# Performance work log

Measured on AMD Instinct MI355X. Metric: run time of the kernel, lower is better.

The kernel has to match this reference:

```python
import jax, jax.numpy as jnp
import numpy as np

N = 100000   # nodes
E = 1600000  # edges
C = 128      # channels
EPS = 1e-5   # BatchNorm eps (PyG gnn.BatchNorm default)


def gcn_conv(x, W, b, src, dst, n):
    """PyG GCNConv: linear -> sym-normalized aggregation with self-loops -> bias."""
    h = x @ W                                      # [N, C]
    # degree with self-loops: in-degree at dst + 1
    deg = jnp.zeros((n,), h.dtype).at[dst].add(jnp.ones((), h.dtype)) + 1.0
    dinv = jax.lax.rsqrt(deg)                      # [N]
    norm = dinv[src] * dinv[dst]                   # [E]
    agg = jnp.zeros_like(h).at[dst].add(h[src] * norm[:, None])
    agg = agg + h * (dinv * dinv)[:, None]         # self-loop contribution
    return agg + b


def batch_norm(x, gamma, beta):
    """Training-mode BatchNorm over the node dimension (per-channel)."""
    mu = jnp.mean(x, axis=0)
    var = jnp.mean(jnp.square(x - mu), axis=0)     # biased variance
    return (x - mu) * jax.lax.rsqrt(var + EPS) * gamma + beta


def setup_inputs() -> dict:
    key = jax.random.key(0)
    ks = jax.random.split(key, 8)
    s = 1.0 / np.sqrt(C)
    x = jax.random.normal(ks[0], (N, C), dtype=jnp.float32)
    edge_index = jax.random.randint(ks[1], (2, E), 0, N, dtype=jnp.int64)
    W1 = jax.random.uniform(ks[2], (C, C), jnp.float32, -s, s)
    b1 = jax.random.uniform(ks[3], (C,), jnp.float32, -s, s)
    W2 = jax.random.uniform(ks[4], (C, C), jnp.float32, -s, s)
    b2 = jax.random.uniform(ks[5], (C,), jnp.float32, -s, s)
    gamma2 = jnp.ones((C,), jnp.float32)
    beta2 = jnp.zeros((C,), jnp.float32)
    return {"x": x, "W1": W1, "b1": b1, "W2": W2, "b2": b2,
            "gamma2": gamma2, "beta2": beta2, "edge_index": edge_index}


def reference(x, W1, b1, W2, b2, gamma2, beta2, edge_index):
    src, dst = edge_index[0], edge_index[1]
    identity = x
    # NOTE: original forward applies batch_norm2 after BOTH convs (batch_norm1 unused).
    h = jax.nn.relu(batch_norm(gcn_conv(x, W1, b1, src, dst, N), gamma2, beta2))
    h = batch_norm(gcn_conv(h, W2, b2, src, dst, N), gamma2, beta2)
    return jax.nn.relu(h + identity)
```

## Files before the change

kernel.cpp:

```cpp
#include <hip/hip_runtime.h>

#define N_NODES 100000
#define EDGES   1600000
#define CH      128
#define BN_EPS  1e-5f

#define BINS     782
#define CHUNKS   256
#define CHUNK_E  (EDGES / CHUNKS)
#define HM       (BINS * CHUNKS)
#define SCAN_NB  (HM / 256)
#define NREP     64

#define GCHUNKS  8
#define GBLKS    (N_NODES / 32)

typedef __attribute__((ext_vector_type(8))) __bf16 bf16x8;
typedef __attribute__((ext_vector_type(4))) __bf16 bf16x4;
typedef __attribute__((ext_vector_type(2))) __bf16 bf16x2;
typedef __attribute__((ext_vector_type(4))) float  f32x4;

__global__ __launch_bounds__(256) void histo_kernel(const int* __restrict__ dst,
                                                    int* __restrict__ histo_g) {
    __shared__ int h[BINS];
    int t = threadIdx.x;
    for (int b = t; b < BINS; b += 256) h[b] = 0;
    __syncthreads();
    int base = blockIdx.x * CHUNK_E;
    for (int i = t; i < CHUNK_E; i += 256)
        atomicAdd(&h[dst[base + i] >> 7], 1);
    __syncthreads();
    for (int b = t; b < BINS; b += 256)
        histo_g[b * CHUNKS + blockIdx.x] = h[b];
}

__global__ __launch_bounds__(256) void scan1(const int* __restrict__ in,
                                             int* __restrict__ scanned,
                                             int* __restrict__ blocksum) {
    __shared__ int sh[2][256];
    int t = threadIdx.x;
    int i = blockIdx.x * 256 + t;
    int v = in[i];
    sh[0][t] = v;
    __syncthreads();
    int pp = 0;
    #pragma unroll
    for (int off = 1; off < 256; off <<= 1) {
        int val = sh[pp][t] + ((t >= off) ? sh[pp][t - off] : 0);
        sh[1 - pp][t] = val;
        pp = 1 - pp;
        __syncthreads();
    }
    int incl = sh[pp][t];
    scanned[i] = incl - v;
    if (t == 255) blocksum[blockIdx.x] = incl;
}

__global__ __launch_bounds__(1024) void scan2(int* __restrict__ blocksum) {
    __shared__ int sh[2][1024];
    int t = threadIdx.x;
    int v = (t < SCAN_NB) ? blocksum[t] : 0;
    sh[0][t] = v;
    __syncthreads();
    int pp = 0;
    #pragma unroll
    for (int off = 1; off < 1024; off <<= 1) {
        int val = sh[pp][t] + ((t >= off) ? sh[pp][t - off] : 0);
        sh[1 - pp][t] = val;
        pp = 1 - pp;
        __syncthreads();
    }
    if (t < SCAN_NB) blocksum[t] = sh[pp][t] - v;
}

__global__ __launch_bounds__(256) void scan3(int* __restrict__ scanned,
                                             const int* __restrict__ blocksum) {
    int i = blockIdx.x * 256 + threadIdx.x;
    scanned[i] += blocksum[blockIdx.x];
    if (i == HM - 1) scanned[HM] = EDGES;
}

__global__ __launch_bounds__(256) void place_kernel(const int* __restrict__ src,
                                                    const int* __restrict__ dst,
                                                    const int* __restrict__ scanned,
                                                    int* __restrict__ binned) {
    __shared__ int cur[BINS];
    int t = threadIdx.x;
    for (int b = t; b < BINS; b += 256)
        cur[b] = scanned[b * CHUNKS + blockIdx.x];
    __syncthreads();
    int base = blockIdx.x * CHUNK_E;
    for (int i = t; i < CHUNK_E; i += 256) {
        int d = dst[base + i];
        int s = src[base + i];
        int pos = atomicAdd(&cur[d >> 7], 1);
        binned[pos] = (s << 7) | (d & 127);
    }
}

__global__ __launch_bounds__(256) void bin_csr(const int* __restrict__ binned,
                                               const int* __restrict__ scanned,
                                               int* __restrict__ srcs,
                                               int* __restrict__ rowptr,
                                               float* __restrict__ dinv) {
    __shared__ int cnt[128];
    __shared__ int sc[2][128];
    __shared__ int base[128];
    __shared__ int cur[128];
    const int t = threadIdx.x;
    const int bin = blockIdx.x;
    if (t < 128) { cnt[t] = 0; cur[t] = 0; }
    __syncthreads();
    const int beg = scanned[bin * CHUNKS];
    const int end = scanned[bin * CHUNKS + CHUNKS];
    for (int e = beg + t; e < end; e += 256)
        atomicAdd(&cnt[binned[e] & 127], 1);
    __syncthreads();
    if (t < 128) sc[0][t] = cnt[t];
    __syncthreads();
    int pp = 0;
    #pragma unroll
    for (int off = 1; off < 128; off <<= 1) {
        if (t < 128) sc[1 - pp][t] = sc[pp][t] + ((t >= off) ? sc[pp][t - off] : 0);
        pp = 1 - pp;
        __syncthreads();
    }
    if (t < 128) {
        base[t] = beg + sc[pp][t] - cnt[t];
        int n = (bin << 7) + t;
        if (n < N_NODES) {
            rowptr[n] = base[t];
            dinv[n] = rsqrtf((float)cnt[t] + 1.0f);
        }
    }
    if (bin == 0 && t == 0) rowptr[N_NODES] = EDGES;
    __syncthreads();
    for (int e = beg + t; e < end; e += 256) {
        int p = binned[e];
        int dl = p & 127;
        int pos = base[dl] + atomicAdd(&cur[dl], 1);
        srcs[pos] = p >> 7;
    }
}

__global__ __launch_bounds__(256) void wtrans2(const float* __restrict__ W1,
                                               __bf16* __restrict__ Wt1,
                                               const float* __restrict__ W2,
                                               __bf16* __restrict__ Wt2,
                                               unsigned* __restrict__ hspad) {
    int b = blockIdx.x;
    if (b == 0 && threadIdx.x < 16) hspad[threadIdx.x] = 0u;
    const float* W = (b < 64) ? W1 : W2;
    __bf16* Wt = (b < 64) ? Wt1 : Wt2;
    int idx = (b & 63) * 256 + threadIdx.x;
    int n = idx >> 7, k = idx & 127;
    Wt[idx] = (__bf16)W[k * 128 + n];
}

__global__ __launch_bounds__(256) void gemm_f32(const float* __restrict__ A,
                                                const __bf16* __restrict__ Wt,
                                                const float* __restrict__ dinv,
                                                __bf16* __restrict__ hs) {
    const int wave = threadIdx.x >> 6;
    const int rt = blockIdx.x * 4 + wave;
    if (rt >= N_NODES / 16) return;
    const int lane = threadIdx.x & 63;
    const int ln = lane & 15;
    const int quad = lane >> 4;
    const int arow = rt * 16 + ln;

    f32x4 acc[8];
    #pragma unroll
    for (int ct = 0; ct < 8; ++ct) acc[ct] = (f32x4){0.f, 0.f, 0.f, 0.f};

    #pragma unroll
    for (int k0 = 0; k0 < 128; k0 += 32) {
        const int k = k0 + quad * 8;
        float4 a0 = *(const float4*)(A + (size_t)arow * CH + k);
        float4 a1 = *(const float4*)(A + (size_t)arow * CH + k + 4);
        bf16x8 af;
        af[0] = (__bf16)a0.x; af[1] = (__bf16)a0.y;
        af[2] = (__bf16)a0.z; af[3] = (__bf16)a0.w;
        af[4] = (__bf16)a1.x; af[5] = (__bf16)a1.y;
        af[6] = (__bf16)a1.z; af[7] = (__bf16)a1.w;
        #pragma unroll
        for (int ct = 0; ct < 8; ++ct) {
            bf16x8 bfrag = *(const bf16x8*)(Wt + (size_t)(ct * 16 + ln) * CH + k);
            acc[ct] = __builtin_amdgcn_mfma_f32_16x16x32_bf16(af, bfrag, acc[ct], 0, 0, 0);
        }
    }

    #pragma unroll
    for (int r = 0; r < 4; ++r) {
        const int row_r = rt * 16 + quad * 4 + r;
        const float dr = dinv[row_r];
        #pragma unroll
        for (int ct = 0; ct < 8; ++ct)
            hs[((size_t)ct * N_NODES + row_r) * 16 + ln] = (__bf16)(acc[ct][r] * dr);
    }
}

__global__ __launch_bounds__(256) void gemm_bn(const __bf16* __restrict__ A,
                                               const __bf16* __restrict__ Wt,
                                               const float* __restrict__ dinv,
                                               const float* __restrict__ scale,
                                               const float* __restrict__ shift,
                                               __bf16* __restrict__ hs) {
    const int wave = threadIdx.x >> 6;
    const int rt = blockIdx.x * 4 + wave;
    if (rt >= N_NODES / 16) return;
    const int lane = threadIdx.x & 63;
    const int ln = lane & 15;
    const int quad = lane >> 4;
    const int arow = rt * 16 + ln;

    f32x4 acc[8];
    #pragma unroll
    for (int ct = 0; ct < 8; ++ct) acc[ct] = (f32x4){0.f, 0.f, 0.f, 0.f};

    #pragma unroll
    for (int k0 = 0; k0 < 128; k0 += 32) {
        const int k = k0 + quad * 8;
        bf16x8 av = *(const bf16x8*)(A + ((size_t)(k >> 4) * N_NODES + arow) * 16 + (k & 15));
        bf16x8 af;
        #pragma unroll
        for (int j = 0; j < 8; ++j)
            af[j] = (__bf16)fmaxf(fmaf((float)av[j], scale[k + j], shift[k + j]), 0.f);
        #pragma unroll
        for (int ct = 0; ct < 8; ++ct) {
            bf16x8 bfrag = *(const bf16x8*)(Wt + (size_t)(ct * 16 + ln) * CH + k);
            acc[ct] = __builtin_amdgcn_mfma_f32_16x16x32_bf16(af, bfrag, acc[ct], 0, 0, 0);
        }
    }

    #pragma unroll
    for (int r = 0; r < 4; ++r) {
        const int row_r = rt * 16 + quad * 4 + r;
        const float dr = dinv[row_r];
        #pragma unroll
        for (int ct = 0; ct < 8; ++ct)
            hs[((size_t)ct * N_NODES + row_r) * 16 + ln] = (__bf16)(acc[ct][r] * dr);
    }
}

__global__ __launch_bounds__(256) void gather_chunk(const __bf16* __restrict__ hs2,
                                                    const int* __restrict__ srcs,
                                                    const int* __restrict__ rowptr,
                                                    const float* __restrict__ dinv,
                                                    __bf16* __restrict__ agg2,
                                                    float* __restrict__ gpart) {
    __shared__ float red[4][8][8][4];
    const int wave = threadIdx.x >> 6;
    const int lane = threadIdx.x & 63;
    const int g  = lane >> 3;
    const int cp = lane & 7;
    const int chunk = blockIdx.x / GBLKS;
    const int nb = blockIdx.x - chunk * GBLKS;
    const unsigned* hp = (const unsigned*)hs2 + (size_t)chunk * (N_NODES * 8);
    const int zidx = (GCHUNKS - chunk) * N_NODES;

    const int n = nb * 32 + wave * 8 + g;
    const int beg = rowptr[n];
    const int end = rowptr[n + 1];
    int dm = end - beg;
    dm = max(dm, __shfl_xor(dm, 8));
    dm = max(dm, __shfl_xor(dm, 16));
    dm = max(dm, __shfl_xor(dm, 32));
    dm = __builtin_amdgcn_readfirstlane(dm);

    bf16x2 s2 = __builtin_bit_cast(bf16x2, hp[(n << 3) + cp]);
    float ax = (float)s2[0], ay = (float)s2[1];

    for (int t0 = 0; t0 < dm; t0 += 8) {
        int e[8];
        #pragma unroll
        for (int u = 0; u < 8; ++u) {
            int jt = beg + t0 + u;
            int sval = srcs[min(jt, EDGES - 1)];
            e[u] = (jt < end) ? sval : zidx;
        }
        unsigned v[8];
        #pragma unroll
        for (int u = 0; u < 8; ++u)
            v[u] = hp[(e[u] << 3) + cp];
        #pragma unroll
        for (int u = 0; u < 8; ++u) {
            bf16x2 b = __builtin_bit_cast(bf16x2, v[u]);
            ax += (float)b[0];
            ay += (float)b[1];
        }
    }

    const float d = dinv[n];
    const float ox = ax * d, oy = ay * d;
    bf16x2 o; o[0] = (__bf16)ox; o[1] = (__bf16)oy;
    ((bf16x2*)agg2 + (size_t)chunk * (N_NODES * 8))[(n << 3) + cp] = o;

    f32x4 rv; rv[0] = ox; rv[1] = ox * ox; rv[2] = oy; rv[3] = oy * oy;
    *(f32x4*)red[wave][g][cp] = rv;
    __syncthreads();
    const int t = threadIdx.x;
    if (t < 32) {
        const int tcp = t >> 2, comp = t & 3;
        float acc = 0.f;
        #pragma unroll
        for (int w = 0; w < 4; ++w)
            #pragma unroll
            for (int gg = 0; gg < 8; ++gg)
                acc += red[w][gg][tcp][comp];
        atomicAdd(&gpart[(blockIdx.x & (NREP - 1)) * 256 + (chunk * 8 + tcp) * 4 + comp], acc);
    }
}

__global__ void bn_final(const float* __restrict__ gpart,
                         const float* __restrict__ gamma,
                         const float* __restrict__ beta,
                         float* __restrict__ scale,
                         float* __restrict__ shift) {
    int c = threadIdx.x;
    int c2 = c >> 1, odd = c & 1;
    float s = 0.f, ss = 0.f;
    for (int r = 0; r < NREP; ++r) {
        s  += gpart[r * 256 + c2 * 4 + 2 * odd];
        ss += gpart[r * 256 + c2 * 4 + 2 * odd + 1];
    }
    const float invN = 1.0f / (float)N_NODES;
    float mu = s * invN;
    float var = ss * invN - mu * mu;
    float sc = gamma[c] * rsqrtf(var + BN_EPS);
    scale[c] = sc;
    shift[c] = beta[c] - mu * sc;
}

__global__ __launch_bounds__(256) void bn_apply_res_relu(const __bf16* __restrict__ v,
                                                         const float* __restrict__ scale,
                                                         const float* __restrict__ shift,
                                                         const float* __restrict__ xin,
                                                         float* __restrict__ outv) {
    int i = blockIdx.x * 256 + threadIdx.x;
    int n = i >> 5, cg = i & 31;
    bf16x4 a4 = *(const bf16x4*)(v + ((size_t)(cg >> 2) * N_NODES + n) * 16 + (cg & 3) * 4);
    float4 r = ((const float4*)xin)[i];
    float4 sc = ((const float4*)scale)[cg];
    float4 sh = ((const float4*)shift)[cg];
    float4 a;
    a.x = fmaxf(fmaf((float)a4[0], sc.x, sh.x) + r.x, 0.f);
    a.y = fmaxf(fmaf((float)a4[1], sc.y, sh.y) + r.y, 0.f);
    a.z = fmaxf(fmaf((float)a4[2], sc.z, sh.z) + r.z, 0.f);
    a.w = fmaxf(fmaf((float)a4[3], sc.w, sh.w) + r.w, 0.f);
    ((float4*)outv)[i] = a;
}

extern "C" void kernel_launch(void* const* d_in, const int* in_sizes, int n_in,
                              void* d_out, int out_size, void* d_ws, size_t ws_size,
                              hipStream_t stream) {
    const float* x      = (const float*)d_in[0];
    const float* W1     = (const float*)d_in[1];
    const float* W2     = (const float*)d_in[3];
    const float* gamma2 = (const float*)d_in[5];
    const float* beta2  = (const float*)d_in[6];
    const int*   ei     = (const int*)d_in[7];
    const int*   srcI   = ei;
    const int*   dstI   = ei + EDGES;
    float* out = (float*)d_out;

    char* ws = (char*)d_ws;
    __bf16*   agg      = (__bf16*)(ws);
    __bf16*   hs       = (__bf16*)(ws + 25600000);
    unsigned* hspad    = (unsigned*)(ws + 51200000);
    int*      binned   = (int*)   (ws + 51200128);
    int*      srcs     = (int*)   (ws + 57600128);
    int*      histo_g  = (int*)   (ws + 64000128);
    int*      scanned  = (int*)   (ws + 64800896);
    int*      blocksum = (int*)   (ws + 65601680);
    float*    dinv     = (float*) (ws + 65604864);
    int*      rowptr   = (int*)   (ws + 66004864);
    __bf16*   Wt1      = (__bf16*)(ws + 66404928);
    __bf16*   Wt2      = (__bf16*)(ws + 66437696);
    float*    gpart    = (float*) (ws + 66470464);
    float*    scale1   = (float*) (ws + 66536000);
    float*    shift1   = scale1 + 128;
    float*    scale2   = scale1 + 256;
    float*    shift2   = scale1 + 384;

    const int ELEM4_BLOCKS  = (N_NODES * 32) / 256;
    const int GEMM_BLOCKS   = (N_NODES / 16 + 3) / 4;
    const int GATHER_BLOCKS = GCHUNKS * GBLKS;

    histo_kernel<<<CHUNKS, 256, 0, stream>>>(dstI, histo_g);
    scan1<<<SCAN_NB, 256, 0, stream>>>(histo_g, scanned, blocksum);
    scan2<<<1, 1024, 0, stream>>>(blocksum);
    scan3<<<SCAN_NB, 256, 0, stream>>>(scanned, blocksum);
    place_kernel<<<CHUNKS, 256, 0, stream>>>(srcI, dstI, scanned, binned);
    bin_csr<<<BINS, 256, 0, stream>>>(binned, scanned, srcs, rowptr, dinv);
    wtrans2<<<128, 256, 0, stream>>>(W1, Wt1, W2, Wt2, hspad);

    gemm_f32<<<GEMM_BLOCKS, 256, 0, stream>>>(x, Wt1, dinv, hs);
    hipMemsetAsync(gpart, 0, NREP * 256 * sizeof(float), stream);
    gather_chunk<<<GATHER_BLOCKS, 256, 0, stream>>>(hs, srcs, rowptr, dinv, agg, gpart);
    bn_final<<<1, 128, 0, stream>>>(gpart, gamma2, beta2, scale1, shift1);

    gemm_bn<<<GEMM_BLOCKS, 256, 0, stream>>>(agg, Wt2, dinv, scale1, shift1, hs);
    hipMemsetAsync(gpart, 0, NREP * 256 * sizeof(float), stream);
    gather_chunk<<<GATHER_BLOCKS, 256, 0, stream>>>(hs, srcs, rowptr, dinv, agg, gpart);
    bn_final<<<1, 128, 0, stream>>>(gpart, gamma2, beta2, scale2, shift2);
    bn_apply_res_relu<<<ELEM4_BLOCKS, 256, 0, stream>>>(agg, scale2, shift2, x, out);
}
```

Measured before the change: 433.7 us.

## Widen feature chunks to 32 channels and restructure gather to parallelize edges per node

The bf16 feature layout changes from 8 chunks of 16 channels to 4 chunks of 32 channels, so each gathered neighbor row is a 64-byte contiguous read. The gather now gives each node a whole wave: 16 lanes cover the channels and 4 slots split the edges, followed by a cross-slot shuffle reduction, instead of one node per 8-lane group padded to the group's max degree. Separately, the scan3 kernel is removed and its block offsets are added directly in place_kernel and bin_csr, saving one launch and one pass over memory. The risks are extra shuffle work per node and edge-index reads that run up to three entries past each row's end.

```diff
diff --git a/kernel.cpp b/kernel.cpp
--- a/kernel.cpp
+++ b/kernel.cpp
@@ -12,8 +12,8 @@
 #define SCAN_NB  (HM / 256)
 #define NREP     64
 
-#define GCHUNKS  8
-#define GBLKS    (N_NODES / 32)
+#define GCHUNKS  4
+#define GBLKS    (N_NODES / 16)
 
 typedef __attribute__((ext_vector_type(8))) __bf16 bf16x8;
 typedef __attribute__((ext_vector_type(4))) __bf16 bf16x4;
@@ -73,21 +73,15 @@
     if (t < SCAN_NB) blocksum[t] = sh[pp][t] - v;
 }
 
-__global__ __launch_bounds__(256) void scan3(int* __restrict__ scanned,
-                                             const int* __restrict__ blocksum) {
-    int i = blockIdx.x * 256 + threadIdx.x;
-    scanned[i] += blocksum[blockIdx.x];
-    if (i == HM - 1) scanned[HM] = EDGES;
-}
-
 __global__ __launch_bounds__(256) void place_kernel(const int* __restrict__ src,
                                                     const int* __restrict__ dst,
                                                     const int* __restrict__ scanned,
+                                                    const int* __restrict__ blocksum,
                                                     int* __restrict__ binned) {
     __shared__ int cur[BINS];
     int t = threadIdx.x;
     for (int b = t; b < BINS; b += 256)
-        cur[b] = scanned[b * CHUNKS + blockIdx.x];
+        cur[b] = scanned[b * CHUNKS + blockIdx.x] + blocksum[b];
     __syncthreads();
     int base = blockIdx.x * CHUNK_E;
     for (int i = t; i < CHUNK_E; i += 256) {
@@ -100,6 +94,7 @@
 
 __global__ __launch_bounds__(256) void bin_csr(const int* __restrict__ binned,
                                                const int* __restrict__ scanned,
+                                               const int* __restrict__ blocksum,
                                                int* __restrict__ srcs,
                                                int* __restrict__ rowptr,
                                                float* __restrict__ dinv) {
@@ -111,8 +106,9 @@
     const int bin = blockIdx.x;
     if (t < 128) { cnt[t] = 0; cur[t] = 0; }
     __syncthreads();
-    const int beg = scanned[bin * CHUNKS];
-    const int end = scanned[bin * CHUNKS + CHUNKS];
+    const int beg = scanned[bin * CHUNKS] + blocksum[bin];
+    const int end = (bin == BINS - 1) ? EDGES
+                    : (scanned[(bin + 1) * CHUNKS] + blocksum[bin + 1]);
     for (int e = beg + t; e < end; e += 256)
         atomicAdd(&cnt[binned[e] & 127], 1);
     __syncthreads();
@@ -196,7 +192,8 @@
         const float dr = dinv[row_r];
         #pragma unroll
         for (int ct = 0; ct < 8; ++ct)
-            hs[((size_t)ct * N_NODES + row_r) * 16 + ln] = (__bf16)(acc[ct][r] * dr);
+            hs[((size_t)(ct >> 1) * N_NODES + row_r) * 32 + (ct & 1) * 16 + ln] =
+                (__bf16)(acc[ct][r] * dr);
     }
 }
 
@@ -221,7 +218,7 @@
     #pragma unroll
     for (int k0 = 0; k0 < 128; k0 += 32) {
         const int k = k0 + quad * 8;
-        bf16x8 av = *(const bf16x8*)(A + ((size_t)(k >> 4) * N_NODES + arow) * 16 + (k & 15));
+        bf16x8 av = *(const bf16x8*)(A + ((size_t)(k >> 5) * N_NODES + arow) * 32 + (k & 31));
         bf16x8 af;
         #pragma unroll
         for (int j = 0; j < 8; ++j)
@@ -239,76 +236,83 @@
         const float dr = dinv[row_r];
         #pragma unroll
         for (int ct = 0; ct < 8; ++ct)
-            hs[((size_t)ct * N_NODES + row_r) * 16 + ln] = (__bf16)(acc[ct][r] * dr);
-    }
-}
-
-__global__ __launch_bounds__(256) void gather_chunk(const __bf16* __restrict__ hs2,
-                                                    const int* __restrict__ srcs,
-                                                    const int* __restrict__ rowptr,
-                                                    const float* __restrict__ dinv,
-                                                    __bf16* __restrict__ agg2,
-                                                    float* __restrict__ gpart) {
-    __shared__ float red[4][8][8][4];
+            hs[((size_t)(ct >> 1) * N_NODES + row_r) * 32 + (ct & 1) * 16 + ln] =
+                (__bf16)(acc[ct][r] * dr);
+    }
+}
+
+__global__ __launch_bounds__(256) void gather_chunk4(const __bf16* __restrict__ hs2,
+                                                     const int* __restrict__ srcs,
+                                                     const int* __restrict__ rowptr,
+                                                     const float* __restrict__ dinv,
+                                                     __bf16* __restrict__ agg2,
+                                                     float* __restrict__ gpart) {
+    __shared__ float red[4][4][16][4];
     const int wave = threadIdx.x >> 6;
     const int lane = threadIdx.x & 63;
-    const int g  = lane >> 3;
-    const int cp = lane & 7;
+    const int slot = lane >> 4;
+    const int cp   = lane & 15;
     const int chunk = blockIdx.x / GBLKS;
-    const int nb = blockIdx.x - chunk * GBLKS;
-    const unsigned* hp = (const unsigned*)hs2 + (size_t)chunk * (N_NODES * 8);
+    const int nb = (blockIdx.x - chunk * GBLKS) * 16 + wave * 4;
+    const unsigned* hp = (const unsigned*)hs2 + (size_t)chunk * (N_NODES * 16);
     const int zidx = (GCHUNKS - chunk) * N_NODES;
 
-    const int n = nb * 32 + wave * 8 + g;
-    const int beg = rowptr[n];
-    const int end = rowptr[n + 1];
-    int dm = end - beg;
-    dm = max(dm, __shfl_xor(dm, 8));
-    dm = max(dm, __shfl_xor(dm, 16));
-    dm = max(dm, __shfl_xor(dm, 32));
-    dm = __builtin_amdgcn_readfirstlane(dm);
-
-    bf16x2 s2 = __builtin_bit_cast(bf16x2, hp[(n << 3) + cp]);
-    float ax = (float)s2[0], ay = (float)s2[1];
-
-    for (int t0 = 0; t0 < dm; t0 += 8) {
-        int e[8];
-        #pragma unroll
-        for (int u = 0; u < 8; ++u) {
-            int jt = beg + t0 + u;
-            int sval = srcs[min(jt, EDGES - 1)];
-            e[u] = (jt < end) ? sval : zidx;
+    unsigned resv = 0u;
+    float bs0 = 0.f, bss0 = 0.f, bs1 = 0.f, bss1 = 0.f;
+
+    #pragma unroll
+    for (int i = 0; i < 4; ++i) {
+        const int n = __builtin_amdgcn_readfirstlane(nb + i);
+        const int beg = rowptr[n];
+        const int deg = rowptr[n + 1] - beg;
+        float ax = 0.f, ay = 0.f;
+        int jp = slot;
+        for (int j = 0; j < deg; j += 4) {
+            const int sj = beg + j;
+            int s0 = srcs[sj + 0];
+            int s1 = srcs[sj + 1];
+            int s2v = srcs[sj + 2];
+            int s3 = srcs[sj + 3];
+            int ea = (slot & 1) ? s1 : s0;
+            int eb = (slot & 1) ? s3 : s2v;
+            int e  = (slot & 2) ? eb : ea;
+            e = (jp < deg) ? e : zidx;
+            unsigned hv = hp[(e << 4) + cp];
+            ax += __builtin_bit_cast(float, hv << 16);
+            ay += __builtin_bit_cast(float, hv & 0xffff0000u);
+            jp += 4;
         }
-        unsigned v[8];
-        #pragma unroll
-        for (int u = 0; u < 8; ++u)
-            v[u] = hp[(e[u] << 3) + cp];
-        #pragma unroll
-        for (int u = 0; u < 8; ++u) {
-            bf16x2 b = __builtin_bit_cast(bf16x2, v[u]);
-            ax += (float)b[0];
-            ay += (float)b[1];
-        }
-    }
-
-    const float d = dinv[n];
-    const float ox = ax * d, oy = ay * d;
-    bf16x2 o; o[0] = (__bf16)ox; o[1] = (__bf16)oy;
-    ((bf16x2*)agg2 + (size_t)chunk * (N_NODES * 8))[(n << 3) + cp] = o;
-
-    f32x4 rv; rv[0] = ox; rv[1] = ox * ox; rv[2] = oy; rv[3] = oy * oy;
-    *(f32x4*)red[wave][g][cp] = rv;
+        ax += __shfl_xor(ax, 16); ax += __shfl_xor(ax, 32);
+        ay += __shfl_xor(ay, 16); ay += __shfl_xor(ay, 32);
+        unsigned sv = hp[(n << 4) + cp];
+        ax += __builtin_bit_cast(float, sv << 16);
+        ay += __builtin_bit_cast(float, sv & 0xffff0000u);
+        const float d = dinv[n];
+        const float ox = ax * d, oy = ay * d;
+        bf16x2 pk; pk[0] = (__bf16)ox; pk[1] = (__bf16)oy;
+        unsigned pv = __builtin_bit_cast(unsigned, pk);
+        resv = (slot == i) ? pv : resv;
+        bs0 += ox; bss0 += ox * ox;
+        bs1 += oy; bss1 += oy * oy;
+    }
+
+    ((unsigned*)agg2)[(size_t)chunk * (N_NODES * 16) + (size_t)nb * 16 + lane] = resv;
+
+    f32x4 rv;
+    rv[0] = bs0 * 0.25f; rv[1] = bss0 * 0.25f;
+    rv[2] = bs1 * 0.25f; rv[3] = bss1 * 0.25f;
+    *(f32x4*)red[wave][slot][cp] = rv;
     __syncthreads();
     const int t = threadIdx.x;
-    if (t < 32) {
+    if (t < 64) {
         const int tcp = t >> 2, comp = t & 3;
         float acc = 0.f;
         #pragma unroll
         for (int w = 0; w < 4; ++w)
             #pragma unroll
-            for (int gg = 0; gg < 8; ++gg)
-                acc += red[w][gg][tcp][comp];
-        atomicAdd(&gpart[(blockIdx.x & (NREP - 1)) * 256 + (chunk * 8 + tcp) * 4 + comp], acc);
+            for (int s = 0; s < 4; ++s)
+                acc += red[w][s][tcp][comp];
+        atomicAdd(&gpart[(blockIdx.x & (NREP - 1)) * 256 + ((chunk * 16 + tcp) << 2) + comp], acc);
     }
 }
 
@@ -339,7 +343,7 @@
                                                          float* __restrict__ outv) {
     int i = blockIdx.x * 256 + threadIdx.x;
     int n = i >> 5, cg = i & 31;
-    bf16x4 a4 = *(const bf16x4*)(v + ((size_t)(cg >> 2) * N_NODES + n) * 16 + (cg & 3) * 4);
+    bf16x4 a4 = *(const bf16x4*)(v + ((size_t)(cg >> 3) * N_NODES + n) * 32 + (cg & 7) * 4);
     float4 r = ((const float4*)xin)[i];
     float4 sc = ((const float4*)scale)[cg];
     float4 sh = ((const float4*)shift)[cg];
@@ -390,19 +394,18 @@
     histo_kernel<<<CHUNKS, 256, 0, stream>>>(dstI, histo_g);
     scan1<<<SCAN_NB, 256, 0, stream>>>(histo_g, scanned, blocksum);
     scan2<<<1, 1024, 0, stream>>>(blocksum);
-    scan3<<<SCAN_NB, 256, 0, stream>>>(scanned, blocksum);
-    place_kernel<<<CHUNKS, 256, 0, stream>>>(srcI, dstI, scanned, binned);
-    bin_csr<<<BINS, 256, 0, stream>>>(binned, scanned, srcs, rowptr, dinv);
+    place_kernel<<<CHUNKS, 256, 0, stream>>>(srcI, dstI, scanned, blocksum, binned);
+    bin_csr<<<BINS, 256, 0, stream>>>(binned, scanned, blocksum, srcs, rowptr, dinv);
     wtrans2<<<128, 256, 0, stream>>>(W1, Wt1, W2, Wt2, hspad);
 
     gemm_f32<<<GEMM_BLOCKS, 256, 0, stream>>>(x, Wt1, dinv, hs);
     hipMemsetAsync(gpart, 0, NREP * 256 * sizeof(float), stream);
-    gather_chunk<<<GATHER_BLOCKS, 256, 0, stream>>>(hs, srcs, rowptr, dinv, agg, gpart);
+    gather_chunk4<<<GATHER_BLOCKS, 256, 0, stream>>>(hs, srcs, rowptr, dinv, agg, gpart);
     bn_final<<<1, 128, 0, stream>>>(gpart, gamma2, beta2, scale1, shift1);
 
     gemm_bn<<<GEMM_BLOCKS, 256, 0, stream>>>(agg, Wt2, dinv, scale1, shift1, hs);
     hipMemsetAsync(gpart, 0, NREP * 256 * sizeof(float), stream);
-    gather_chunk<<<GATHER_BLOCKS, 256, 0, stream>>>(hs, srcs, rowptr, dinv, agg, gpart);
+    gather_chunk4<<<GATHER_BLOCKS, 256, 0, stream>>>(hs, srcs, rowptr, dinv, agg, gpart);
     bn_final<<<1, 128, 0, stream>>>(gpart, gamma2, beta2, scale2, shift2);
     bn_apply_res_relu<<<ELEM4_BLOCKS, 256, 0, stream>>>(agg, scale2, shift2, x, out);
 }
```

After: 519.8 us. 19.9% more time.
